# Performance work log

Hardware: AMD Instinct MI355X
Metric: run time of the kernel (lower is better)

Reference implementation:

```python
import jax, jax.numpy as jnp
import numpy as np

EPS = 1e-5  # BatchNorm eps; BN applied in eval mode with running_mean=0, running_var=1


def conv1x1(x, w, b=None):
    # x: [B,C,H,W], w: [O,C] -> [B,O,H,W]
    y = jnp.einsum('bchw,oc->bohw', x, w)
    if b is not None:
        y = y + b[None, :, None, None]
    return y


def bn_eval(x, gamma, beta):
    # running_mean=0, running_var=1
    scale = gamma / jnp.sqrt(1.0 + EPS)
    return x * scale[None, :, None, None] + beta[None, :, None, None]


def glnl_forward(x, mask, wt_nl, bt_nl, wp_nl, bp_nl, wt_l, bt_l, wp_l, bp_l,
                 wg_nl, bg_nl, wg_l, bg_l, wW, bW, gW, betaW, wWl, gWl, betaWl):
    B, C, H, W = x.shape
    I = wt_nl.shape[0]
    N = H * W

    # non-local branch score [B,N,N]
    th_nl = conv1x1(x, wt_nl, bt_nl).reshape(B, I, N)
    ph_nl = conv1x1(x, wp_nl, bp_nl).reshape(B, I, N)
    score_nl = jax.nn.softmax(jnp.einsum('bin,bim->bnm', th_nl, ph_nl), axis=-1)

    # local branch: mask-gated projections, score [B,N,N]
    m = mask.reshape(B, 1, N)
    th_l = conv1x1(x, wt_l, bt_l).reshape(B, I, N) * m
    ph_l = conv1x1(x, wp_l, bp_l).reshape(B, I, N) * m
    score_l = jax.nn.softmax(jnp.einsum('bin,bim->bnm', th_l, ph_l), axis=-1)

    # value projections [B,I,N]
    g_nl = conv1x1(x, wg_nl, bg_nl).reshape(B, I, N)
    g_l = conv1x1(x, wg_l, bg_l).reshape(B, I, N)

    # attention aggregation -> [B,I,H,W]
    y_nl = jnp.einsum('bnm,bim->bin', score_nl, g_nl).reshape(B, I, H, W)
    y_l = jnp.einsum('bnm,bim->bin', score_l, g_l).reshape(B, I, H, W)

    # W_local: conv1x1 (no bias) -> ReLU -> BN
    y_l = bn_eval(jax.nn.relu(conv1x1(y_l, wWl)), gWl, betaWl)

    y = y_nl + y_l
    # W: conv1x1 -> ReLU -> BN, then residual
    W_y = bn_eval(jax.nn.relu(conv1x1(y, wW, bW)), gW, betaW)
    return W_y + x


def setup_inputs() -> dict:
    key = jax.random.key(0)
    ks = jax.random.split(key, 20)
    B, C, I, H, W = 4, 128, 64, 64, 64
    s = 0.02
    inp = {
        'x': jax.random.normal(ks[0], (B, C, H, W), jnp.float32),
        'mask': (jax.random.uniform(ks[1], (B, 1, H, W)) > 0.5).astype(jnp.float32),
        'wt_nl': jax.random.normal(ks[2], (I, C)) * s, 'bt_nl': jnp.zeros((I,)),
        'wp_nl': jax.random.normal(ks[3], (I, C)) * s, 'bp_nl': jnp.zeros((I,)),
        'wt_l': jax.random.normal(ks[4], (I, C)) * s, 'bt_l': jnp.zeros((I,)),
        'wp_l': jax.random.normal(ks[5], (I, C)) * s, 'bp_l': jnp.zeros((I,)),
        'wg_nl': jax.random.normal(ks[6], (I, C)) * s, 'bg_nl': jnp.zeros((I,)),
        'wg_l': jax.random.normal(ks[7], (I, C)) * s, 'bg_l': jnp.zeros((I,)),
        'wW': jax.random.normal(ks[8], (C, I)) * s, 'bW': jnp.zeros((C,)),
        'gW': jnp.ones((C,)), 'betaW': jnp.zeros((C,)),
        'wWl': jax.random.normal(ks[9], (I, I)) * s,
        'gWl': jnp.ones((I,)), 'betaWl': jnp.zeros((I,)),
    }
    return inp


def reference(x, mask, wt_nl, bt_nl, wp_nl, bp_nl, wt_l, bt_l, wp_l, bp_l,
              wg_nl, bg_nl, wg_l, bg_l, wW, bW, gW, betaW, wWl, gWl, betaWl):
    return glnl_forward(x, mask, wt_nl, bt_nl, wp_nl, bp_nl, wt_l, bt_l, wp_l, bp_l,
                        wg_nl, bg_nl, wg_l, bg_l, wW, bW, gW, betaW, wWl, gWl, betaWl)
```

## Files before the change

kernel.cpp:

```cpp
#include <hip/hip_runtime.h>

typedef unsigned short u16;
typedef __attribute__((ext_vector_type(8))) short short8;
typedef __attribute__((ext_vector_type(4))) float floatx4;

#define MFMA16(a, b, c) __builtin_amdgcn_mfma_f32_16x16x32_bf16((a), (b), (c), 0, 0, 0)

#define SZ_P ((size_t)4 * 64 * 4096)

__device__ __forceinline__ float bf2f(u16 u) {
    union { unsigned int i; float f; } v; v.i = ((unsigned int)u) << 16; return v.f;
}
__device__ __forceinline__ u16 f2bf(float f) {
    union { float f; unsigned int i; } v; v.f = f;
    unsigned int r = v.i + 0x7fffu + ((v.i >> 16) & 1u);
    return (u16)(r >> 16);
}
__device__ __forceinline__ unsigned int pk2(float a, float b) {
    union { float f; unsigned int u; } x, y; x.f = a; y.f = b;
    return (x.u >> 16) | (y.u & 0xffff0000u);
}

__global__ __launch_bounds__(256) void k_prep_w(
    const float* __restrict__ w0, const float* __restrict__ w1,
    const float* __restrict__ w2, const float* __restrict__ w3,
    const float* __restrict__ w4, const float* __restrict__ w5,
    const float* __restrict__ wWl, const float* __restrict__ wW,
    u16* __restrict__ wbf)
{
    const int idx = blockIdx.x * 256 + threadIdx.x;
    float v;
    if (idx < 49152) {
        const int j = idx >> 13, off = idx & 8191;
        const float* s = (j == 0) ? w0 : (j == 1) ? w1 : (j == 2) ? w2
                       : (j == 3) ? w3 : (j == 4) ? w4 : w5;
        v = s[off];
    } else if (idx < 53248) {
        v = wWl[idx - 49152];
    } else {
        v = wW[idx - 53248];
    }
    wbf[idx] = f2bf(v);
}

__global__ __launch_bounds__(256) void k_proj(
    const float* __restrict__ x, const float* __restrict__ mask,
    const u16* __restrict__ wbf,
    const float* __restrict__ bq0f, const float* __restrict__ bk0f,
    const float* __restrict__ bv0f,
    const float* __restrict__ bq1f, const float* __restrict__ bk1f,
    const float* __restrict__ bv1f,
    u16* __restrict__ q0, u16* __restrict__ k0, u16* __restrict__ v0,
    u16* __restrict__ q1, u16* __restrict__ k1, u16* __restrict__ v1)
{
    __shared__ __align__(16) u16 xt_s[64 * 136];
    const int n0 = blockIdx.x * 64, b = blockIdx.y;
    const int br = blockIdx.z >> 1, half = blockIdx.z & 1;
    const u16* wq = wbf + br * 24576;
    const u16* wk = wq + 8192;
    const u16* wv = wk + 8192;
    const float* bq = br ? bq1f : bq0f;
    const float* bk = br ? bk1f : bk0f;
    const float* bv = br ? bv1f : bv0f;
    u16* q = br ? q1 : q0;  u16* k = br ? k1 : k0;  u16* v = br ? v1 : v0;

    const int t = threadIdx.x, w = t >> 6, lane = t & 63;
    const int quad = lane >> 4, l15 = lane & 15;
    const float* xb = x + ((size_t)b << 19);

    for (int idx = t; idx < 8192; idx += 256) {
        const int c = idx >> 6, n = idx & 63;
        xt_s[n * 136 + c] = f2bf(xb[((size_t)c << 12) + n0 + n]);
    }
    __syncthreads();

    short8 ax[4];
#pragma unroll
    for (int cc = 0; cc < 4; ++cc)
        ax[cc] = *(const short8*)&xt_s[(w * 16 + l15) * 136 + quad * 8 + cc * 32];

    float mv[4] = {1.f, 1.f, 1.f, 1.f};
    if (br) {
#pragma unroll
        for (int r = 0; r < 4; ++r)
            mv[r] = mask[((size_t)b << 12) + n0 + w * 16 + quad * 4 + r];
    }

#pragma unroll
    for (int qk = 0; qk < 2; ++qk) {
        const u16* wsel = qk ? wk : wq;
        const float* bb = qk ? bk : bq;
        u16* o = qk ? k : q;
#pragma unroll
        for (int nsh = 0; nsh < 2; ++nsh) {
            const int ns = half * 2 + nsh;
            floatx4 acc = {0.f, 0.f, 0.f, 0.f};
            const u16* wp = wsel + (ns * 16 + l15) * 128 + quad * 8;
#pragma unroll
            for (int cc = 0; cc < 4; ++cc)
                acc = MFMA16(ax[cc], *(const short8*)(wp + cc * 32), acc);
            const float bias_i = bb[ns * 16 + l15];
#pragma unroll
            for (int r = 0; r < 4; ++r) {
                const float val = (acc[r] + bias_i) * mv[r];
                o[((size_t)b << 18) + (size_t)(n0 + w * 16 + quad * 4 + r) * 64
                  + ns * 16 + l15] = f2bf(val);
            }
        }
    }

    short8 aw[4];
#pragma unroll
    for (int cc = 0; cc < 4; ++cc)
        aw[cc] = *(const short8*)(wv + (w * 16 + l15) * 128 + quad * 8 + cc * 32);
    float bvr[4];
#pragma unroll
    for (int r = 0; r < 4; ++r) bvr[r] = bv[w * 16 + quad * 4 + r];
#pragma unroll
    for (int nsh = 0; nsh < 2; ++nsh) {
        const int ns = half * 2 + nsh;
        floatx4 acc = {0.f, 0.f, 0.f, 0.f};
#pragma unroll
        for (int cc = 0; cc < 4; ++cc)
            acc = MFMA16(aw[cc],
                *(const short8*)&xt_s[(ns * 16 + l15) * 136 + quad * 8 + cc * 32], acc);
#pragma unroll
        for (int r = 0; r < 4; ++r) {
            v[((size_t)b << 18) + ((size_t)(w * 16 + quad * 4 + r) << 12)
              + n0 + ns * 16 + l15] = f2bf(acc[r] + bvr[r]);
        }
    }
}

__global__ __launch_bounds__(256) void k_flash(
    const u16* __restrict__ Q0, const u16* __restrict__ K0,
    const u16* __restrict__ V0,
    const u16* __restrict__ Q1, const u16* __restrict__ K1,
    const u16* __restrict__ V1,
    u16* __restrict__ num, float* __restrict__ den)
{
    __shared__ __align__(16) u16 kt_s[2][64 * 72];
    __shared__ __align__(16) u16 vt_s[2][64 * 72];
    __shared__ __align__(16) u16 p_s[4 * 32 * 72];

    const int flat = blockIdx.x;
    const int g = flat & 15, tile = flat >> 4;
    const int b = g >> 2, z = g & 3;
    const int br = z >> 1, sp = z & 1;
    const int qb = tile * 128;
    const size_t base = ((size_t)b << 18);
    const u16* Q = (br ? Q1 : Q0) + base;
    const u16* K = (br ? K1 : K0) + base;
    const u16* V = (br ? V1 : V0) + base;
    u16* numo = num + (size_t)z * SZ_P + base;
    float* deno = den + z * 16384 + b * 4096;

    const int t = threadIdx.x, w = t >> 6, lane = t & 63;
    const int quad = lane >> 4, l15 = lane & 15;
    const int pw = w * 32 * 72;

    const int r0 = t >> 3, r1 = (t + 256) >> 3, cg8 = (t & 7) * 8;
    const u16* Kp0 = K + (size_t)r0 * 64 + cg8;
    const u16* Kp1 = K + (size_t)r1 * 64 + cg8;
    const u16* Vp0 = V + ((size_t)r0 << 12) + cg8;
    const u16* Vp1 = V + ((size_t)r1 << 12) + cg8;
    const int lk0 = r0 * 72 + cg8, lk1 = r1 * 72 + cg8;

    short8 aq[2][2];
#pragma unroll
    for (int t2 = 0; t2 < 2; ++t2)
#pragma unroll
        for (int s = 0; s < 2; ++s)
            aq[t2][s] = *(const short8*)(Q + (size_t)(qb + w * 32 + t2 * 16 + l15) * 64
                                         + s * 32 + quad * 8);

    const short8 ones8 = {0x3F80, 0x3F80, 0x3F80, 0x3F80, 0x3F80, 0x3F80, 0x3F80, 0x3F80};

    floatx4 oacc[4][2];
#pragma unroll
    for (int it = 0; it < 4; ++it)
#pragma unroll
        for (int t2 = 0; t2 < 2; ++t2) oacc[it][t2] = (floatx4){0.f, 0.f, 0.f, 0.f};
    floatx4 lacc[2] = {{0.f, 0.f, 0.f, 0.f}, {0.f, 0.f, 0.f, 0.f}};

    const int roff = tile & 31;
    const int m_beg = sp * 2048;

    {
        const int m0 = m_beg + (roff << 6);
        *(short8*)&kt_s[0][lk0] = *(const short8*)(Kp0 + (size_t)m0 * 64);
        *(short8*)&kt_s[0][lk1] = *(const short8*)(Kp1 + (size_t)m0 * 64);
        *(short8*)&vt_s[0][lk0] = *(const short8*)(Vp0 + m0);
        *(short8*)&vt_s[0][lk1] = *(const short8*)(Vp1 + m0);
    }

    for (int j = 0; j < 32; ++j) {
        const int cur = j & 1;
        const int mn = m_beg + (((roff + j + 1) & 31) << 6);
        short8 pk0v = *(const short8*)(Kp0 + (size_t)mn * 64);
        short8 pk1v = *(const short8*)(Kp1 + (size_t)mn * 64);
        short8 pv0v = *(const short8*)(Vp0 + mn);
        short8 pv1v = *(const short8*)(Vp1 + mn);
        __syncthreads();

#pragma unroll
        for (int mt = 0; mt < 4; ++mt) {
            const u16* kp = &kt_s[cur][(mt * 16 + l15) * 72 + quad * 8];
            const short8 ka0 = *(const short8*)kp;
            const short8 ka1 = *(const short8*)(kp + 32);
#pragma unroll
            for (int t2 = 0; t2 < 2; ++t2) {
                floatx4 acc = {0.f, 0.f, 0.f, 0.f};
                acc = MFMA16(ka0, aq[t2][0], acc);
                acc = MFMA16(ka1, aq[t2][1], acc);
                const float e0 = __expf(acc[0]), e1 = __expf(acc[1]);
                const float e2 = __expf(acc[2]), e3 = __expf(acc[3]);
                *(uint2*)&p_s[pw + (t2 * 16 + l15) * 72 + mt * 16 + quad * 4] =
                    make_uint2(pk2(e0, e1), pk2(e2, e3));
            }
        }

        short8 pb2[2][2];
#pragma unroll
        for (int t2 = 0; t2 < 2; ++t2)
#pragma unroll
            for (int s = 0; s < 2; ++s)
                pb2[t2][s] = *(const short8*)&p_s[pw + (t2 * 16 + l15) * 72 + s * 32 + quad * 8];
#pragma unroll
        for (int it = 0; it < 4; ++it) {
            const u16* vp = &vt_s[cur][(it * 16 + l15) * 72 + quad * 8];
            const short8 va0 = *(const short8*)vp;
            const short8 va1 = *(const short8*)(vp + 32);
#pragma unroll
            for (int t2 = 0; t2 < 2; ++t2) {
                oacc[it][t2] = MFMA16(va0, pb2[t2][0], oacc[it][t2]);
                oacc[it][t2] = MFMA16(va1, pb2[t2][1], oacc[it][t2]);
            }
        }
#pragma unroll
        for (int t2 = 0; t2 < 2; ++t2) {
            lacc[t2] = MFMA16(ones8, pb2[t2][0], lacc[t2]);
            lacc[t2] = MFMA16(ones8, pb2[t2][1], lacc[t2]);
        }

        *(short8*)&kt_s[cur ^ 1][lk0] = pk0v;
        *(short8*)&kt_s[cur ^ 1][lk1] = pk1v;
        *(short8*)&vt_s[cur ^ 1][lk0] = pv0v;
        *(short8*)&vt_s[cur ^ 1][lk1] = pv1v;
    }

    if (quad == 0) {
#pragma unroll
        for (int t2 = 0; t2 < 2; ++t2)
            deno[qb + w * 32 + t2 * 16 + l15] = lacc[t2][0];
    }

#pragma unroll
    for (int it = 0; it < 4; ++it)
#pragma unroll
        for (int t2 = 0; t2 < 2; ++t2) {
            *(uint2*)&p_s[pw + (t2 * 16 + l15) * 72 + it * 16 + quad * 4] =
                make_uint2(pk2(oacc[it][t2][0], oacc[it][t2][1]),
                           pk2(oacc[it][t2][2], oacc[it][t2][3]));
        }
    __syncthreads();
#pragma unroll
    for (int ch = t; ch < 1024; ch += 256) {
        const int row = ch >> 3, cg = ch & 7;
        *(short8*)(numo + (size_t)(qb + row) * 64 + cg * 8) =
            *(const short8*)&p_s[(row >> 5) * 2304 + (row & 31) * 72 + cg * 8];
    }
}

__global__ __launch_bounds__(256) void k_epi(
    const u16* __restrict__ num, const float* __restrict__ den,
    const u16* __restrict__ wbf,
    const float* __restrict__ gWl, const float* __restrict__ betaWl,
    const float* __restrict__ bW, const float* __restrict__ gW,
    const float* __restrict__ betaW,
    const float* __restrict__ x, float* __restrict__ out)
{
    __shared__ __align__(16) u16 yl_s[16 * 72];
    __shared__ __align__(16) u16 ynl_s[16 * 72];
    __shared__ __align__(16) u16 yy_s[16 * 72];
    const int b = blockIdx.y, n0 = blockIdx.x * 16;
    const int t = threadIdx.x, w = t >> 6, lane = t & 63;
    const int quad = lane >> 4, l15 = lane & 15;
    const size_t ybase = ((size_t)b << 18) + (size_t)n0 * 64;

    if (t < 128) {
        const int row = t >> 3, cg = t & 7;
        const float dn = den[b * 4096 + n0 + row] + den[16384 + b * 4096 + n0 + row];
        const float dl = den[32768 + b * 4096 + n0 + row] + den[49152 + b * 4096 + n0 + row];
        const float inl = 1.0f / dn, ilo = 1.0f / dl;
        const short8 a0 = *(const short8*)(num + ybase + row * 64 + cg * 8);
        const short8 a1 = *(const short8*)(num + SZ_P + ybase + row * 64 + cg * 8);
        const short8 c0 = *(const short8*)(num + 2 * SZ_P + ybase + row * 64 + cg * 8);
        const short8 c1 = *(const short8*)(num + 3 * SZ_P + ybase + row * 64 + cg * 8);
        short8 ynl8, yl8;
#pragma unroll
        for (int j = 0; j < 8; ++j) {
            ynl8[j] = (short)f2bf((bf2f((u16)a0[j]) + bf2f((u16)a1[j])) * inl);
            yl8[j]  = (short)f2bf((bf2f((u16)c0[j]) + bf2f((u16)c1[j])) * ilo);
        }
        *(short8*)&ynl_s[row * 72 + cg * 8] = ynl8;
        *(short8*)&yl_s[row * 72 + cg * 8] = yl8;
    }
    __syncthreads();
    const float rsq = rsqrtf(1.0f + 1e-5f);
    const u16* wblW = wbf + 49152;
    const u16* wbW  = wbf + 53248;

    {
        const short8 a0 = *(const short8*)(wblW + (w * 16 + l15) * 64 + quad * 8);
        const short8 a1 = *(const short8*)(wblW + (w * 16 + l15) * 64 + 32 + quad * 8);
        float sc[4], bt[4];
#pragma unroll
        for (int r = 0; r < 4; ++r) {
            const int io = w * 16 + quad * 4 + r;
            sc[r] = gWl[io] * rsq;
            bt[r] = betaWl[io];
        }
        floatx4 acc = {0.f, 0.f, 0.f, 0.f};
        const u16* bp_ = &yl_s[l15 * 72 + quad * 8];
        acc = MFMA16(a0, *(const short8*)bp_, acc);
        acc = MFMA16(a1, *(const short8*)(bp_ + 32), acc);
#pragma unroll
        for (int r = 0; r < 4; ++r) {
            const int io = w * 16 + quad * 4 + r;
            float val = fmaxf(acc[r], 0.f) * sc[r] + bt[r];
            val += bf2f(ynl_s[l15 * 72 + io]);
            yy_s[l15 * 72 + io] = f2bf(val);
        }
    }
    __syncthreads();

#pragma unroll
    for (int rb = 0; rb < 2; ++rb) {
        const int c0 = rb * 64 + w * 16;
        const short8 a0 = *(const short8*)(wbW + (c0 + l15) * 64 + quad * 8);
        const short8 a1 = *(const short8*)(wbW + (c0 + l15) * 64 + 32 + quad * 8);
        float bs[4], sc[4], bt[4];
#pragma unroll
        for (int r = 0; r < 4; ++r) {
            const int c = c0 + quad * 4 + r;
            bs[r] = bW[c];
            sc[r] = gW[c] * rsq;
            bt[r] = betaW[c];
        }
        floatx4 acc = {0.f, 0.f, 0.f, 0.f};
        const u16* bp_ = &yy_s[l15 * 72 + quad * 8];
        acc = MFMA16(a0, *(const short8*)bp_, acc);
        acc = MFMA16(a1, *(const short8*)(bp_ + 32), acc);
#pragma unroll
        for (int r = 0; r < 4; ++r) {
            const int c = c0 + quad * 4 + r;
            float val = fmaxf(acc[r] + bs[r], 0.f) * sc[r] + bt[r];
            const size_t xi = ((size_t)b << 19) + ((size_t)c << 12) + n0 + l15;
            out[xi] = val + x[xi];
        }
    }
}

extern "C" void kernel_launch(void* const* d_in, const int* in_sizes, int n_in,
                              void* d_out, int out_size, void* d_ws, size_t ws_size,
                              hipStream_t stream) {
    const float* x      = (const float*)d_in[0];
    const float* mask   = (const float*)d_in[1];
    const float* wt_nl  = (const float*)d_in[2];  const float* bt_nl = (const float*)d_in[3];
    const float* wp_nl  = (const float*)d_in[4];  const float* bp_nl = (const float*)d_in[5];
    const float* wt_l   = (const float*)d_in[6];  const float* bt_l  = (const float*)d_in[7];
    const float* wp_l   = (const float*)d_in[8];  const float* bp_l  = (const float*)d_in[9];
    const float* wg_nl  = (const float*)d_in[10]; const float* bg_nl = (const float*)d_in[11];
    const float* wg_l   = (const float*)d_in[12]; const float* bg_l  = (const float*)d_in[13];
    const float* wW     = (const float*)d_in[14]; const float* bW    = (const float*)d_in[15];
    const float* gW     = (const float*)d_in[16]; const float* betaW = (const float*)d_in[17];
    const float* wWl    = (const float*)d_in[18]; const float* gWl   = (const float*)d_in[19];
    const float* betaWl = (const float*)d_in[20];

    u16* ws  = (u16*)d_ws;
    u16* wbf = ws;
    u16* q0  = wbf + 61440;
    u16* k0  = q0 + SZ_P;
    u16* v0  = k0 + SZ_P;
    u16* q1  = v0 + SZ_P;
    u16* k1  = q1 + SZ_P;
    u16* v1  = k1 + SZ_P;
    u16* num = v1 + SZ_P;
    float* den = (float*)(num + 4 * SZ_P);

    k_prep_w<<<dim3(240), 256, 0, stream>>>(wt_nl, wp_nl, wg_nl,
                                            wt_l, wp_l, wg_l, wWl, wW, wbf);
    k_proj<<<dim3(64, 4, 4), 256, 0, stream>>>(x, mask, wbf,
        bt_nl, bp_nl, bg_nl, bt_l, bp_l, bg_l,
        q0, k0, v0, q1, k1, v1);
    k_flash<<<dim3(512), 256, 0, stream>>>(q0, k0, v0, q1, k1, v1, num, den);
    k_epi<<<dim3(256, 4), 256, 0, stream>>>(num, den, wbf, gWl, betaWl,
                                            bW, gW, betaW, x, (float*)d_out);
}
```

Before: 180.6 us.

## Split flash attention into 4 key splits with 512-thread blocks and exp2

```diff
diff --git a/kernel.cpp b/kernel.cpp
--- a/kernel.cpp
+++ b/kernel.cpp
@@ -1,10 +1,12 @@
 #include <hip/hip_runtime.h>
+#include <hip/hip_bf16.h>
 
 typedef unsigned short u16;
 typedef __attribute__((ext_vector_type(8))) short short8;
 typedef __attribute__((ext_vector_type(4))) float floatx4;
 
 #define MFMA16(a, b, c) __builtin_amdgcn_mfma_f32_16x16x32_bf16((a), (b), (c), 0, 0, 0)
+#define LOG2E 1.44269504088896340736f
 
 #define SZ_P ((size_t)4 * 64 * 4096)
 
@@ -17,8 +19,9 @@
     return (u16)(r >> 16);
 }
 __device__ __forceinline__ unsigned int pk2(float a, float b) {
-    union { float f; unsigned int u; } x, y; x.f = a; y.f = b;
-    return (x.u >> 16) | (y.u & 0xffff0000u);
+    union { __hip_bfloat162 h; unsigned int u; } v;
+    v.h = __float22bfloat162_rn(make_float2(a, b));
+    return v.u;
 }
 
 __global__ __launch_bounds__(256) void k_prep_w(
@@ -91,6 +94,7 @@
         const u16* wsel = qk ? wk : wq;
         const float* bb = qk ? bk : bq;
         u16* o = qk ? k : q;
+        const float qscale = qk ? 1.0f : LOG2E;
 #pragma unroll
         for (int nsh = 0; nsh < 2; ++nsh) {
             const int ns = half * 2 + nsh;
@@ -102,7 +106,7 @@
             const float bias_i = bb[ns * 16 + l15];
 #pragma unroll
             for (int r = 0; r < 4; ++r) {
-                const float val = (acc[r] + bias_i) * mv[r];
+                const float val = (acc[r] + bias_i) * mv[r] * qscale;
                 o[((size_t)b << 18) + (size_t)(n0 + w * 16 + quad * 4 + r) * 64
                   + ns * 16 + l15] = f2bf(val);
             }
@@ -132,7 +136,7 @@
     }
 }
 
-__global__ __launch_bounds__(256) void k_flash(
+__global__ __launch_bounds__(512, 4) void k_flash(
     const u16* __restrict__ Q0, const u16* __restrict__ K0,
     const u16* __restrict__ V0,
     const u16* __restrict__ Q1, const u16* __restrict__ K1,
@@ -141,13 +145,13 @@
 {
     __shared__ __align__(16) u16 kt_s[2][64 * 72];
     __shared__ __align__(16) u16 vt_s[2][64 * 72];
-    __shared__ __align__(16) u16 p_s[4 * 32 * 72];
+    __shared__ __align__(16) u16 p_s[8 * 32 * 72];
 
     const int flat = blockIdx.x;
-    const int g = flat & 15, tile = flat >> 4;
-    const int b = g >> 2, z = g & 3;
-    const int br = z >> 1, sp = z & 1;
-    const int qb = tile * 128;
+    const int g = flat & 31, tile = flat >> 5;
+    const int b = g >> 3, br = (g >> 2) & 1, sp = g & 3;
+    const int z = br * 4 + sp;
+    const int qb = tile * 256;
     const size_t base = ((size_t)b << 18);
     const u16* Q = (br ? Q1 : Q0) + base;
     const u16* K = (br ? K1 : K0) + base;
@@ -159,12 +163,10 @@
     const int quad = lane >> 4, l15 = lane & 15;
     const int pw = w * 32 * 72;
 
-    const int r0 = t >> 3, r1 = (t + 256) >> 3, cg8 = (t & 7) * 8;
+    const int r0 = t >> 3, cg8 = (t & 7) * 8;
     const u16* Kp0 = K + (size_t)r0 * 64 + cg8;
-    const u16* Kp1 = K + (size_t)r1 * 64 + cg8;
     const u16* Vp0 = V + ((size_t)r0 << 12) + cg8;
-    const u16* Vp1 = V + ((size_t)r1 << 12) + cg8;
-    const int lk0 = r0 * 72 + cg8, lk1 = r1 * 72 + cg8;
+    const int lk0 = r0 * 72 + cg8;
 
     short8 aq[2][2];
 #pragma unroll
@@ -174,33 +176,27 @@
             aq[t2][s] = *(const short8*)(Q + (size_t)(qb + w * 32 + t2 * 16 + l15) * 64
                                          + s * 32 + quad * 8);
 
-    const short8 ones8 = {0x3F80, 0x3F80, 0x3F80, 0x3F80, 0x3F80, 0x3F80, 0x3F80, 0x3F80};
-
     floatx4 oacc[4][2];
 #pragma unroll
     for (int it = 0; it < 4; ++it)
 #pragma unroll
         for (int t2 = 0; t2 < 2; ++t2) oacc[it][t2] = (floatx4){0.f, 0.f, 0.f, 0.f};
-    floatx4 lacc[2] = {{0.f, 0.f, 0.f, 0.f}, {0.f, 0.f, 0.f, 0.f}};
-
-    const int roff = tile & 31;
-    const int m_beg = sp * 2048;
+    float dacc[2] = {0.f, 0.f};
+
+    const int roff = tile & 15;
+    const int m_beg = sp * 1024;
 
     {
         const int m0 = m_beg + (roff << 6);
         *(short8*)&kt_s[0][lk0] = *(const short8*)(Kp0 + (size_t)m0 * 64);
-        *(short8*)&kt_s[0][lk1] = *(const short8*)(Kp1 + (size_t)m0 * 64);
         *(short8*)&vt_s[0][lk0] = *(const short8*)(Vp0 + m0);
-        *(short8*)&vt_s[0][lk1] = *(const short8*)(Vp1 + m0);
-    }
-
-    for (int j = 0; j < 32; ++j) {
+    }
+
+    for (int j = 0; j < 16; ++j) {
         const int cur = j & 1;
-        const int mn = m_beg + (((roff + j + 1) & 31) << 6);
-        short8 pk0v = *(const short8*)(Kp0 + (size_t)mn * 64);
-        short8 pk1v = *(const short8*)(Kp1 + (size_t)mn * 64);
-        short8 pv0v = *(const short8*)(Vp0 + mn);
-        short8 pv1v = *(const short8*)(Vp1 + mn);
+        const int mn = m_beg + (((roff + j + 1) & 15) << 6);
+        short8 pkv = *(const short8*)(Kp0 + (size_t)mn * 64);
+        short8 pvv = *(const short8*)(Vp0 + mn);
         __syncthreads();
 
 #pragma unroll
@@ -213,8 +209,9 @@
                 floatx4 acc = {0.f, 0.f, 0.f, 0.f};
                 acc = MFMA16(ka0, aq[t2][0], acc);
                 acc = MFMA16(ka1, aq[t2][1], acc);
-                const float e0 = __expf(acc[0]), e1 = __expf(acc[1]);
-                const float e2 = __expf(acc[2]), e3 = __expf(acc[3]);
+                const float e0 = exp2f(acc[0]), e1 = exp2f(acc[1]);
+                const float e2 = exp2f(acc[2]), e3 = exp2f(acc[3]);
+                dacc[t2] += (e0 + e1) + (e2 + e3);
                 *(uint2*)&p_s[pw + (t2 * 16 + l15) * 72 + mt * 16 + quad * 4] =
                     make_uint2(pk2(e0, e1), pk2(e2, e3));
             }
@@ -237,22 +234,17 @@
                 oacc[it][t2] = MFMA16(va1, pb2[t2][1], oacc[it][t2]);
             }
         }
-#pragma unroll
-        for (int t2 = 0; t2 < 2; ++t2) {
-            lacc[t2] = MFMA16(ones8, pb2[t2][0], lacc[t2]);
-            lacc[t2] = MFMA16(ones8, pb2[t2][1], lacc[t2]);
-        }
-
-        *(short8*)&kt_s[cur ^ 1][lk0] = pk0v;
-        *(short8*)&kt_s[cur ^ 1][lk1] = pk1v;
-        *(short8*)&vt_s[cur ^ 1][lk0] = pv0v;
-        *(short8*)&vt_s[cur ^ 1][lk1] = pv1v;
-    }
-
-    if (quad == 0) {
-#pragma unroll
-        for (int t2 = 0; t2 < 2; ++t2)
-            deno[qb + w * 32 + t2 * 16 + l15] = lacc[t2][0];
+
+        *(short8*)&kt_s[cur ^ 1][lk0] = pkv;
+        *(short8*)&vt_s[cur ^ 1][lk0] = pvv;
+    }
+
+#pragma unroll
+    for (int t2 = 0; t2 < 2; ++t2) {
+        float d = dacc[t2];
+        d += __shfl_xor(d, 16, 64);
+        d += __shfl_xor(d, 32, 64);
+        if (quad == 0) deno[qb + w * 32 + t2 * 16 + l15] = d;
     }
 
 #pragma unroll
@@ -265,7 +257,7 @@
         }
     __syncthreads();
 #pragma unroll
-    for (int ch = t; ch < 1024; ch += 256) {
+    for (int ch = t; ch < 2048; ch += 512) {
         const int row = ch >> 3, cg = ch & 7;
         *(short8*)(numo + (size_t)(qb + row) * 64 + cg * 8) =
             *(const short8*)&p_s[(row >> 5) * 2304 + (row & 31) * 72 + cg * 8];
@@ -290,18 +282,29 @@
 
     if (t < 128) {
         const int row = t >> 3, cg = t & 7;
-        const float dn = den[b * 4096 + n0 + row] + den[16384 + b * 4096 + n0 + row];
-        const float dl = den[32768 + b * 4096 + n0 + row] + den[49152 + b * 4096 + n0 + row];
+        float dn = 0.f, dl = 0.f;
+#pragma unroll
+        for (int sp = 0; sp < 4; ++sp) {
+            dn += den[sp * 16384 + b * 4096 + n0 + row];
+            dl += den[(4 + sp) * 16384 + b * 4096 + n0 + row];
+        }
         const float inl = 1.0f / dn, ilo = 1.0f / dl;
-        const short8 a0 = *(const short8*)(num + ybase + row * 64 + cg * 8);
-        const short8 a1 = *(const short8*)(num + SZ_P + ybase + row * 64 + cg * 8);
-        const short8 c0 = *(const short8*)(num + 2 * SZ_P + ybase + row * 64 + cg * 8);
-        const short8 c1 = *(const short8*)(num + 3 * SZ_P + ybase + row * 64 + cg * 8);
+        float an[8] = {0, 0, 0, 0, 0, 0, 0, 0}, al[8] = {0, 0, 0, 0, 0, 0, 0, 0};
+#pragma unroll
+        for (int sp = 0; sp < 4; ++sp) {
+            const short8 vn = *(const short8*)(num + (size_t)sp * SZ_P + ybase + row * 64 + cg * 8);
+            const short8 vl = *(const short8*)(num + (size_t)(4 + sp) * SZ_P + ybase + row * 64 + cg * 8);
+#pragma unroll
+            for (int j = 0; j < 8; ++j) {
+                an[j] += bf2f((u16)vn[j]);
+                al[j] += bf2f((u16)vl[j]);
+            }
+        }
         short8 ynl8, yl8;
 #pragma unroll
         for (int j = 0; j < 8; ++j) {
-            ynl8[j] = (short)f2bf((bf2f((u16)a0[j]) + bf2f((u16)a1[j])) * inl);
-            yl8[j]  = (short)f2bf((bf2f((u16)c0[j]) + bf2f((u16)c1[j])) * ilo);
+            ynl8[j] = (short)f2bf(an[j] * inl);
+            yl8[j]  = (short)f2bf(al[j] * ilo);
         }
         *(short8*)&ynl_s[row * 72 + cg * 8] = ynl8;
         *(short8*)&yl_s[row * 72 + cg * 8] = yl8;
@@ -387,14 +390,14 @@
     u16* k1  = q1 + SZ_P;
     u16* v1  = k1 + SZ_P;
     u16* num = v1 + SZ_P;
-    float* den = (float*)(num + 4 * SZ_P);
+    float* den = (float*)(num + 8 * SZ_P);
 
     k_prep_w<<<dim3(240), 256, 0, stream>>>(wt_nl, wp_nl, wg_nl,
                                             wt_l, wp_l, wg_l, wWl, wW, wbf);
     k_proj<<<dim3(64, 4, 4), 256, 0, stream>>>(x, mask, wbf,
         bt_nl, bp_nl, bg_nl, bt_l, bp_l, bg_l,
         q0, k0, v0, q1, k1, v1);
-    k_flash<<<dim3(512), 256, 0, stream>>>(q0, k0, v0, q1, k1, v1, num, den);
+    k_flash<<<dim3(512), 512, 0, stream>>>(q0, k0, v0, q1, k1, v1, num, den);
     k_epi<<<dim3(256, 4), 256, 0, stream>>>(num, den, wbf, gWl, betaWl,
                                             bW, gW, betaW, x, (float*)d_out);
 }
```

Measured after the change: 179.7 us. About the same (-0.5%).
